# Optimization experiments

Measured on AMD Instinct MI355X. Metric: run time of the kernel, lower is better.

The kernel has to match this reference:

```python
import jax, jax.numpy as jnp
import numpy as np

NUM_EMBEDDINGS = 8192
EMBEDDING_DIM = 256


def setup_inputs() -> dict:
    key = jax.random.key(0)
    kx, kw = jax.random.split(key)
    x = jax.random.normal(kx, (16384, EMBEDDING_DIM), dtype=jnp.float32)
    # nn.Embedding weight initialized uniform(-1/K, 1/K)
    bound = 1.0 / NUM_EMBEDDINGS
    weight = jax.random.uniform(kw, (NUM_EMBEDDINGS, EMBEDDING_DIM),
                                dtype=jnp.float32, minval=-bound, maxval=bound)
    return {"x": x, "weight": weight}


def reference(x, weight):
    # flatten to (N, D)
    flat_x = x.reshape(-1, EMBEDDING_DIM)
    distances = (jnp.sum(flat_x * flat_x, axis=1, keepdims=True)
                 + jnp.sum(weight * weight, axis=1)
                 - 2.0 * jnp.matmul(flat_x, weight.T))
    encoding_indices = jnp.argmin(distances, axis=1)  # (N,)
    quantized = weight[encoding_indices].reshape(x.shape)
    return quantized, encoding_indices
```

## Files before the change

kernel.cpp:

```cpp
#include <hip/hip_runtime.h>
#include <hip/hip_bf16.h>

#define NROWS 16384
#define NCODES 8192
#define DIM 256
#define BM 128
#define SPLITS 2
#define CPB (NCODES / SPLITS)
#define CAP 24
#define MARGIN 3.0e-4f

#define WFRAG_BLOCKS 1024
#define SQ_BLOCKS 1536

typedef __attribute__((ext_vector_type(8))) short bf16x8;
typedef __attribute__((ext_vector_type(4))) float f32x4;

__device__ inline unsigned short f2bf(float f) {
    union { __hip_bfloat16 h; unsigned short u; } cv;
    cv.h = __float2bfloat16(f);
    return cv.u;
}
__device__ inline unsigned f2ord(float f) {
    unsigned u = __float_as_uint(f);
    return u ^ ((u >> 31) ? 0xFFFFFFFFu : 0x80000000u);
}
__device__ inline float ord2f(unsigned u) {
    unsigned v = (u & 0x80000000u) ? (u ^ 0x80000000u) : ~u;
    return __uint_as_float(v);
}

__global__ __launch_bounds__(256)
void prep_kernel(const float* __restrict__ x, const float* __restrict__ w,
                 unsigned short* __restrict__ whf,
                 float* __restrict__ xsq, float* __restrict__ wsq,
                 unsigned long long* __restrict__ best64g) {
    if (blockIdx.x < WFRAG_BLOCKS) {
        int tid = blockIdx.x * 256 + threadIdx.x;
        int L = tid & 63;
        int rest = tid >> 6;
        int c16 = rest & 511;
        int k32 = rest >> 9;
        int code = c16 * 16 + (L & 15);
        int k = k32 * 32 + (L >> 4) * 8;
        const float4* p = reinterpret_cast<const float4*>(w + (size_t)code * DIM + k);
        float4 u0 = p[0], u1 = p[1];
        unsigned short tmp[8];
        tmp[0] = f2bf(u0.x); tmp[1] = f2bf(u0.y); tmp[2] = f2bf(u0.z); tmp[3] = f2bf(u0.w);
        tmp[4] = f2bf(u1.x); tmp[5] = f2bf(u1.y); tmp[6] = f2bf(u1.z); tmp[7] = f2bf(u1.w);
        *reinterpret_cast<uint4*>(whf + (size_t)tid * 8) = *reinterpret_cast<uint4*>(tmp);
    } else {
        int blk = blockIdx.x - WFRAG_BLOCKS;
        int row = blk * 16 + (threadIdx.x >> 4);
        int c = threadIdx.x & 15;
        int j = c & 7, h = c >> 3;
        const float* src = (row < NROWS) ? (x + (size_t)row * DIM)
                                         : (w + (size_t)(row - NROWS) * DIM);
        const float* base = src + h * 128 + j;
        float r = 0.0f;
        #pragma unroll
        for (int g = 0; g < 16; ++g) {
            float v = base[g * 8];
            r = __fadd_rn(r, __fmul_rn(v, v));
        }
        float t;
        t = __shfl_xor(r, 1, 64); r = __fadd_rn(r, t);
        t = __shfl_xor(r, 2, 64); r = __fadd_rn(r, t);
        t = __shfl_xor(r, 4, 64); r = __fadd_rn(r, t);
        t = __shfl_xor(r, 8, 64); r = __fadd_rn(r, t);
        if (c == 0) {
            if (row < NROWS) xsq[row] = r;
            else wsq[row - NROWS] = r;
        }
        if (c == 1 && row < NROWS) best64g[row] = 0xFFFFFFFFFFFFFFFFULL;
    }
}

__global__ __launch_bounds__(512, 2)
void vq_main(const float* __restrict__ x, const float* __restrict__ w,
             const unsigned short* __restrict__ whf,
             const float* __restrict__ wsq, const float* __restrict__ xsq,
             unsigned long long* __restrict__ best64g) {
    __shared__ unsigned short afrag[8 * 8 * 64 * 8];
    __shared__ unsigned rowmin[BM];
    __shared__ int cnt[BM];
    __shared__ int cand[BM][CAP];

    const int tid = threadIdx.x;
    const int lane = tid & 63;
    const int wv = tid >> 6;
    const int lm = lane & 15;
    const int lq = lane >> 4;

    const int blk = blockIdx.x;
    const int xcd = blk & 7;
    const int split = xcd & 1;
    const int rowGroup = (xcd >> 1) * 32 + (blk >> 3);
    const int rowBase = rowGroup * BM;
    const int codeBase = split * CPB;

    if (tid < BM) { rowmin[tid] = 0xFFFFFFFFu; cnt[tid] = 0; }

    {
        const int rg = wv;
        const float* xr = x + (size_t)(rowBase + rg * 16 + lm) * DIM + lq * 8;
        #pragma unroll
        for (int k32 = 0; k32 < 8; ++k32) {
            float4 u0 = *reinterpret_cast<const float4*>(xr + k32 * 32);
            float4 u1 = *reinterpret_cast<const float4*>(xr + k32 * 32 + 4);
            unsigned short t8[8];
            t8[0] = f2bf(u0.x); t8[1] = f2bf(u0.y); t8[2] = f2bf(u0.z); t8[3] = f2bf(u0.w);
            t8[4] = f2bf(u1.x); t8[5] = f2bf(u1.y); t8[6] = f2bf(u1.z); t8[7] = f2bf(u1.w);
            *reinterpret_cast<uint4*>(afrag + ((rg * 8 + k32) * 64 + lane) * 8) =
                *reinterpret_cast<uint4*>(t8);
        }
    }
    __syncthreads();

    const int waveCode16 = (codeBase >> 4) + wv * 32;

    for (int p = 0; p < 8; ++p) {
        const int pbase16 = waveCode16 + p * 4;
        f32x4 acc[8][4];
        #pragma unroll
        for (int rg = 0; rg < 8; ++rg)
            #pragma unroll
            for (int cf = 0; cf < 4; ++cf)
                acc[rg][cf] = (f32x4){0.f, 0.f, 0.f, 0.f};

        float wq[4][4];
        #pragma unroll
        for (int cf = 0; cf < 4; ++cf)
            #pragma unroll
            for (int r = 0; r < 4; ++r)
                wq[cf][r] = wsq[(pbase16 + cf) * 16 + lq * 4 + r];

        bf16x8 bb[2][4];
        #pragma unroll
        for (int cf = 0; cf < 4; ++cf)
            bb[0][cf] = *reinterpret_cast<const bf16x8*>(
                whf + (((size_t)(pbase16 + cf)) * 64 + lane) * 8);

        #pragma unroll
        for (int k32 = 0; k32 < 8; ++k32) {
            const int cur = k32 & 1;
            if (k32 < 7) {
                #pragma unroll
                for (int cf = 0; cf < 4; ++cf)
                    bb[cur ^ 1][cf] = *reinterpret_cast<const bf16x8*>(
                        whf + (((size_t)((k32 + 1) * 512 + pbase16 + cf)) * 64 + lane) * 8);
            }
            bf16x8 a[8];
            #pragma unroll
            for (int rg = 0; rg < 8; ++rg)
                a[rg] = *reinterpret_cast<const bf16x8*>(
                    afrag + ((rg * 8 + k32) * 64 + lane) * 8);
            #pragma unroll
            for (int cf = 0; cf < 4; ++cf)
                #pragma unroll
                for (int rg = 0; rg < 8; ++rg)
                    acc[rg][cf] = __builtin_amdgcn_mfma_f32_16x16x32_bf16(
                        bb[cur][cf], a[rg], acc[rg][cf], 0, 0, 0);
        }

        float mloc[8];
        #pragma unroll
        for (int rg = 0; rg < 8; ++rg) {
            float mpl = __builtin_huge_valf();
            #pragma unroll
            for (int cf = 0; cf < 4; ++cf)
                #pragma unroll
                for (int r = 0; r < 4; ++r)
                    mpl = fminf(mpl, fmaf(-2.f, acc[rg][cf][r], wq[cf][r]));
            mloc[rg] = mpl;
            float rm = fminf(mpl, __shfl_xor(mpl, 16, 64));
            rm = fminf(rm, __shfl_xor(rm, 32, 64));
            if (lq == 0)
                atomicMin(&rowmin[rg * 16 + lm], f2ord(rm));
        }
        #pragma unroll
        for (int rg = 0; rg < 8; ++rg) {
            const int row = rg * 16 + lm;
            float limit = ord2f(rowmin[row]) + MARGIN;
            if (mloc[rg] <= limit) {
                #pragma unroll
                for (int cf = 0; cf < 4; ++cf)
                    #pragma unroll
                    for (int r = 0; r < 4; ++r) {
                        float s = fmaf(-2.f, acc[rg][cf][r], wq[cf][r]);
                        if (s <= limit) {
                            int pos = atomicAdd(&cnt[row], 1);
                            if (pos < CAP)
                                cand[row][pos] = (pbase16 + cf) * 16 + lq * 4 + r;
                        }
                    }
            }
        }
    }
    __syncthreads();

    for (int slot = tid; slot < BM * CAP; slot += 512) {
        int row = slot / CAP, pos = slot - (slot / CAP) * CAP;
        int n = cnt[row] < CAP ? cnt[row] : CAP;
        if (pos < n) {
            int c = cand[row][pos];
            const float* xr = x + (size_t)(rowBase + row) * DIM;
            const float* wr = w + (size_t)c * DIM;
            float d = 0.f;
            for (int k = 0; k < DIM; k += 4) {
                float4 a = *reinterpret_cast<const float4*>(xr + k);
                float4 b = *reinterpret_cast<const float4*>(wr + k);
                d = fmaf(a.x, b.x, d);
                d = fmaf(a.y, b.y, d);
                d = fmaf(a.z, b.z, d);
                d = fmaf(a.w, b.w, d);
            }
            float t1 = __fadd_rn(xsq[rowBase + row], wsq[c]);
            float s = __fsub_rn(t1, __fadd_rn(d, d));
            unsigned long long key =
                ((unsigned long long)__float_as_uint(s) << 32) | (unsigned)c;
            atomicMin(best64g + rowBase + row, key);
        }
    }
}

__global__ __launch_bounds__(256)
void out_kernel(const float* __restrict__ w,
                const unsigned long long* __restrict__ best64g,
                float* __restrict__ out_q, float* __restrict__ out_idx) {
    int r = blockIdx.x * 4 + (threadIdx.x >> 6);
    int lane = threadIdx.x & 63;
    unsigned long long key = best64g[r];
    int idx = (int)(key & 0xFFFFFFFFu);
    float4 v = reinterpret_cast<const float4*>(w + (size_t)idx * DIM)[lane];
    reinterpret_cast<float4*>(out_q + (size_t)r * DIM)[lane] = v;
    if (lane == 0) out_idx[r] = (float)idx;
}

extern "C" void kernel_launch(void* const* d_in, const int* in_sizes, int n_in,
                              void* d_out, int out_size, void* d_ws, size_t ws_size,
                              hipStream_t stream) {
    const float* x = (const float*)d_in[0];
    const float* w = (const float*)d_in[1];
    float* out_q = (float*)d_out;
    float* out_idx = (float*)d_out + (size_t)NROWS * DIM;

    unsigned short* whf = (unsigned short*)d_ws;
    float* wsq = (float*)((char*)d_ws + (size_t)NCODES * DIM * 2);
    float* xsq = wsq + NCODES;
    unsigned long long* best64g = (unsigned long long*)(xsq + NROWS);

    prep_kernel<<<WFRAG_BLOCKS + SQ_BLOCKS, 256, 0, stream>>>(x, w, whf, xsq, wsq, best64g);
    vq_main<<<(NROWS / BM) * SPLITS, 512, 0, stream>>>(x, w, whf, wsq, xsq, best64g);
    out_kernel<<<NROWS / 4, 256, 0, stream>>>(w, best64g, out_q, out_idx);
}
```

Measured before the change: 229.8 us.

## Filter candidates on raw dot products and reorder weight fragment layout

The candidate prefilter now tracks the maximum raw dot product per row instead of the minimum of wsq − 2·dot. This drops the per-pass wsq loads and the fma work, and merges the min and select loops into one. The margin changes to a dot-product margin, relying on the tiny weight norms being negligible. The bf16 weight fragments are re-laid out so each pass reads contiguous memory, and the fragment addressing is simplified. The risk is that skipping the wsq term in the filter could miss true argmin candidates when norms differ, and that rowmax is read without a barrier after the atomics.

```diff
diff --git a/kernel.cpp b/kernel.cpp
--- a/kernel.cpp
+++ b/kernel.cpp
@@ -8,7 +8,7 @@
 #define SPLITS 2
 #define CPB (NCODES / SPLITS)
 #define CAP 24
-#define MARGIN 3.0e-4f
+#define MARGIND 1.7e-4f
 
 #define WFRAG_BLOCKS 1024
 #define SQ_BLOCKS 1536
@@ -39,8 +39,8 @@
         int tid = blockIdx.x * 256 + threadIdx.x;
         int L = tid & 63;
         int rest = tid >> 6;
-        int c16 = rest & 511;
-        int k32 = rest >> 9;
+        int k32 = rest & 7;
+        int c16 = rest >> 3;
         int code = c16 * 16 + (L & 15);
         int k = k32 * 32 + (L >> 4) * 8;
         const float4* p = reinterpret_cast<const float4*>(w + (size_t)code * DIM + k);
@@ -82,7 +82,7 @@
              const float* __restrict__ wsq, const float* __restrict__ xsq,
              unsigned long long* __restrict__ best64g) {
     __shared__ unsigned short afrag[8 * 8 * 64 * 8];
-    __shared__ unsigned rowmin[BM];
+    __shared__ unsigned rowmax[BM];
     __shared__ int cnt[BM];
     __shared__ int cand[BM][CAP];
 
@@ -99,7 +99,7 @@
     const int rowBase = rowGroup * BM;
     const int codeBase = split * CPB;
 
-    if (tid < BM) { rowmin[tid] = 0xFFFFFFFFu; cnt[tid] = 0; }
+    if (tid < BM) { rowmax[tid] = 0u; cnt[tid] = 0; }
 
     {
         const int rg = wv;
@@ -117,10 +117,13 @@
     }
     __syncthreads();
 
+    const unsigned short* afb = afrag + lane * 8;
     const int waveCode16 = (codeBase >> 4) + wv * 32;
 
     for (int p = 0; p < 8; ++p) {
         const int pbase16 = waveCode16 + p * 4;
+        const unsigned short* wpass = whf + (size_t)pbase16 * 4096 + lane * 8;
+
         f32x4 acc[8][4];
         #pragma unroll
         for (int rg = 0; rg < 8; ++rg)
@@ -128,18 +131,10 @@
             for (int cf = 0; cf < 4; ++cf)
                 acc[rg][cf] = (f32x4){0.f, 0.f, 0.f, 0.f};
 
-        float wq[4][4];
+        bf16x8 bb[2][4];
         #pragma unroll
         for (int cf = 0; cf < 4; ++cf)
-            #pragma unroll
-            for (int r = 0; r < 4; ++r)
-                wq[cf][r] = wsq[(pbase16 + cf) * 16 + lq * 4 + r];
-
-        bf16x8 bb[2][4];
-        #pragma unroll
-        for (int cf = 0; cf < 4; ++cf)
-            bb[0][cf] = *reinterpret_cast<const bf16x8*>(
-                whf + (((size_t)(pbase16 + cf)) * 64 + lane) * 8);
+            bb[0][cf] = *reinterpret_cast<const bf16x8*>(wpass + cf * 4096);
 
         #pragma unroll
         for (int k32 = 0; k32 < 8; ++k32) {
@@ -148,13 +143,12 @@
                 #pragma unroll
                 for (int cf = 0; cf < 4; ++cf)
                     bb[cur ^ 1][cf] = *reinterpret_cast<const bf16x8*>(
-                        whf + (((size_t)((k32 + 1) * 512 + pbase16 + cf)) * 64 + lane) * 8);
+                        wpass + cf * 4096 + (k32 + 1) * 512);
             }
             bf16x8 a[8];
             #pragma unroll
             for (int rg = 0; rg < 8; ++rg)
-                a[rg] = *reinterpret_cast<const bf16x8*>(
-                    afrag + ((rg * 8 + k32) * 64 + lane) * 8);
+                a[rg] = *reinterpret_cast<const bf16x8*>(afb + (rg * 8 + k32) * 512);
             #pragma unroll
             for (int cf = 0; cf < 4; ++cf)
                 #pragma unroll
@@ -163,32 +157,25 @@
                         bb[cur][cf], a[rg], acc[rg][cf], 0, 0, 0);
         }
 
-        float mloc[8];
         #pragma unroll
         for (int rg = 0; rg < 8; ++rg) {
-            float mpl = __builtin_huge_valf();
+            float m = -__builtin_huge_valf();
             #pragma unroll
             for (int cf = 0; cf < 4; ++cf)
                 #pragma unroll
                 for (int r = 0; r < 4; ++r)
-                    mpl = fminf(mpl, fmaf(-2.f, acc[rg][cf][r], wq[cf][r]));
-            mloc[rg] = mpl;
-            float rm = fminf(mpl, __shfl_xor(mpl, 16, 64));
-            rm = fminf(rm, __shfl_xor(rm, 32, 64));
-            if (lq == 0)
-                atomicMin(&rowmin[rg * 16 + lm], f2ord(rm));
-        }
-        #pragma unroll
-        for (int rg = 0; rg < 8; ++rg) {
+                    m = fmaxf(m, acc[rg][cf][r]);
+            float rm = fmaxf(m, __shfl_xor(m, 16, 64));
+            rm = fmaxf(rm, __shfl_xor(rm, 32, 64));
             const int row = rg * 16 + lm;
-            float limit = ord2f(rowmin[row]) + MARGIN;
-            if (mloc[rg] <= limit) {
+            if (lq == 0) atomicMax(&rowmax[row], f2ord(rm));
+            float limit = ord2f(rowmax[row]) - MARGIND;
+            if (m >= limit) {
                 #pragma unroll
                 for (int cf = 0; cf < 4; ++cf)
                     #pragma unroll
                     for (int r = 0; r < 4; ++r) {
-                        float s = fmaf(-2.f, acc[rg][cf][r], wq[cf][r]);
-                        if (s <= limit) {
+                        if (acc[rg][cf][r] >= limit) {
                             int pos = atomicAdd(&cnt[row], 1);
                             if (pos < CAP)
                                 cand[row][pos] = (pbase16 + cf) * 16 + lq * 4 + r;
```

Measured after the change: 226.3 us. About the same (-1.5%).
